# Performance work log

Hardware: AMD Instinct MI355X
Metric: run time of the kernel (lower is better)

## Reference

```python
import jax, jax.numpy as jnp
import numpy as np

DIM, HID, E, K = 512, 2048, 8, 2

def setup_inputs() -> dict:
    key = jax.random.key(0)
    ks = jax.random.split(key, 6)
    x = jax.random.normal(ks[0], (8, 4096, DIM), dtype=jnp.float32)
    assign = jax.random.randint(ks[1], (8, 4096, K), 0, E, dtype=jnp.int32)
    W1 = jax.random.normal(ks[2], (E, DIM, HID), dtype=jnp.float32) * 0.02
    b1 = jnp.zeros((E, HID), dtype=jnp.float32)
    W2 = jax.random.normal(ks[3], (E, HID, DIM), dtype=jnp.float32) * 0.02
    b2 = jnp.zeros((E, DIM), dtype=jnp.float32)
    return {"x": x, "assign": assign, "W1": W1, "b1": b1, "W2": W2, "b2": b2}

def reference(x, assign, W1, b1, W2, b2):
    # x: [B,S,D]; assign: [B,S,K] expert ids; hash router => uniform weights 1/K
    B, S, D = x.shape
    k = assign.shape[-1]
    num_experts = W1.shape[0]
    flat_x = x.reshape(B * S, D)
    flat_assign = assign.reshape(B * S, k)
    inv_k = jnp.asarray(1.0 / k, dtype=x.dtype)
    out = jnp.zeros((B * S, D), dtype=x.dtype)
    for e in range(num_experts):  # small fixed expert count
        # total routing weight for this expert per token (handles duplicate slots)
        token_w = (flat_assign == e).sum(-1).astype(x.dtype) * inv_k  # [B*S]
        h = jax.nn.relu(flat_x @ W1[e] + b1[e])        # [B*S, hidden]
        y = h @ W2[e] + b2[e]                          # [B*S, D]
        out = out + y * token_w[:, None]               # zero weight => zero contribution
    return out.reshape(B, S, D)
```

## Files before the change

kernel.cpp:

```cpp
#include <hip/hip_runtime.h>


#define NTOK 32768
#define DIM  512
#define HID  2048
#define NE   8
#define TM   64
#define MAXTILE 128

#define XBASE 0
#define HBASE 65536
#define RBASE 98304
#define LDS_BYTES 163840

typedef __attribute__((ext_vector_type(8))) short short8;
typedef __attribute__((ext_vector_type(4))) float f32x4;
typedef unsigned short ushort_t;

__device__ __forceinline__ unsigned short f2bf(float f) {
  union { float f; unsigned u; } v; v.f = f;
  unsigned r = v.u + 0x7FFFu + ((v.u >> 16) & 1u);
  return (unsigned short)(r >> 16);
}
__device__ __forceinline__ void g2l16(const void* g, void* l) {
  __builtin_amdgcn_global_load_lds(
      (const __attribute__((address_space(1))) void*)g,
      (__attribute__((address_space(3))) void*)l, 16, 0, 0);
}

#define SCHB __builtin_amdgcn_sched_barrier(0)
#define VMW4 do { asm volatile("s_waitcnt vmcnt(4)" ::: "memory"); SCHB; } while (0)
#define MFMA16(a, b, c) __builtin_amdgcn_mfma_f32_16x16x32_bf16(a, b, c, 0, 0, 0)

__device__ __forceinline__ void transp_body(const float* __restrict__ src,
                                            ushort_t* __restrict__ dst,
                                            int R, int C, int rb, int cb,
                                            int t, float tile[64][68]) {
  {
    const int tr = t >> 2, tc = (t & 3) * 16;
    const f32x4* s = (const f32x4*)(src + (size_t)(rb + tr) * C + cb + tc);
    f32x4 v0 = __builtin_nontemporal_load(s + 0);
    f32x4 v1 = __builtin_nontemporal_load(s + 1);
    f32x4 v2 = __builtin_nontemporal_load(s + 2);
    f32x4 v3 = __builtin_nontemporal_load(s + 3);
    *(f32x4*)&tile[tr][tc + 0]  = v0;
    *(f32x4*)&tile[tr][tc + 4]  = v1;
    *(f32x4*)&tile[tr][tc + 8]  = v2;
    *(f32x4*)&tile[tr][tc + 12] = v3;
  }
  __syncthreads();
  {
    const int n = t >> 2, ks = (t & 3) * 16;
    short8 o0, o1;
#pragma unroll
    for (int j = 0; j < 8; ++j) o0[j] = (short)f2bf(tile[ks + j][n]);
#pragma unroll
    for (int j = 0; j < 8; ++j) o1[j] = (short)f2bf(tile[ks + 8 + j][n]);
    ushort_t* d = dst + (size_t)(cb + n) * R + rb + ks;
    *(short8*)(d) = o0;
    *(short8*)(d + 8) = o1;
  }
}

__global__ __launch_bounds__(256) void moe_prep(
    const float* __restrict__ W1, const float* __restrict__ W2,
    ushort_t* __restrict__ W1b, ushort_t* __restrict__ W2b,
    const int* __restrict__ assign, int* __restrict__ cnt,
    int* __restrict__ lists) {
  __shared__ float tile[64][68];
  __shared__ int lcnt[NE], gbase[NE];
  const int b = blockIdx.x;
  const int t = threadIdx.x;
  if (b < 2048) {
    int e = b >> 8, rem = b & 255;
    int rb = (rem >> 5) * 64, cb = (rem & 31) * 64;
    transp_body(W1 + (size_t)e * DIM * HID, W1b + (size_t)e * HID * DIM,
                DIM, HID, rb, cb, t, tile);
  } else if (b < 4096) {
    int bb = b - 2048;
    int e = bb >> 8, rem = bb & 255;
    int rb = (rem >> 3) * 64, cb = (rem & 7) * 64;
    transp_body(W2 + (size_t)e * HID * DIM, W2b + (size_t)e * DIM * HID,
                HID, DIM, rb, cb, t, tile);
  } else {
    int tt = (b - 4096) * 256 + t;
    if (t < NE) lcnt[t] = 0;
    __syncthreads();
    int a0 = assign[2 * tt + 0];
    int a1 = assign[2 * tt + 1];
    int r0, r1 = -1;
    r0 = atomicAdd(&lcnt[a0], 1);
    if (a0 != a1) r1 = atomicAdd(&lcnt[a1], 1);
    __syncthreads();
    if (t < NE) gbase[t] = atomicAdd(&cnt[t], lcnt[t]);
    __syncthreads();
    if (a0 == a1) {
      lists[a0 * NTOK + gbase[a0] + r0] = tt | 0x10000;
    } else {
      lists[a0 * NTOK + gbase[a0] + r0] = tt;
      lists[a1 * NTOK + gbase[a1] + r1] = tt;
    }
  }
}

__global__ __launch_bounds__(512, 2) void moe_gemm(
    const float* __restrict__ x, const ushort_t* __restrict__ W1b,
    const float* __restrict__ b1, const ushort_t* __restrict__ W2b,
    const float* __restrict__ b2, const int* __restrict__ cnt,
    const int* __restrict__ lists, float* __restrict__ out) {
  extern __shared__ char smem[];

  const int id = blockIdx.x;
  const int e = id & 7;
  const int tile = id >> 3;
  const int n_e = cnt[e];
  const int t0 = tile * TM;
  if (t0 >= n_e) return;

  const int tid = threadIdx.x;
  const int wid = tid >> 6;
  const int lane = tid & 63;
  const int lr = lane & 15, lg = lane >> 4;
  const int lr7 = lr & 7;
  const int lrq = (lr >> 1) & 3;
  const int l3 = lane >> 3, l7 = lane & 7;

  char* const ring0 = smem + RBASE + wid * 8192;

  const ushort_t* gW1c = W1b + ((size_t)(e * HID) + wid * 32 + l3) * DIM + (l7 ^ l3) * 8;
  const ushort_t* gW2c = W2b + ((size_t)(e * DIM) + wid * 64 + (lane >> 2)) * HID +
                         ((lane & 3) ^ ((lane >> 3) & 3)) * 8;
  const float* b1e = b1 + (size_t)e * HID + wid * 32 + lr;

  auto IS_G1 = [&](const ushort_t* wb, int p, int half, int slot) {
    char* d = ring0 + slot * 2048 + lane * 16;
    const ushort_t* g = wb + (size_t)(half * 16) * DIM + p * 64;
    g2l16(g, d);
    g2l16(g + (size_t)8 * DIM, d + 1024);
  };
  auto IS_G2 = [&](const ushort_t* wb, int q, int h, int slot) {
    char* d = ring0 + slot * 2048 + lane * 16;
    const ushort_t* g = wb + (size_t)(h * 32) * HID + q * 32;
    g2l16(g, d);
    g2l16(g + (size_t)16 * HID, d + 1024);
  };

#define B1LOAD(d0, d1, BI) do { \
  const float* a_ = b1e + (BI) * 256; \
  asm volatile("global_load_dword %0, %2, off\n\t" \
               "global_load_dword %1, %2, off offset:64" \
               : "=&v"(d0), "=&v"(d1) : "v"(a_)); \
} while (0)

#define XRD(dst, mf, p, kf) do { \
  const int row_ = (mf) * 16 + lr; \
  const int u_ = (p) * 8 + (kf) * 4 + lg; \
  dst = *(const short8*)(smem + XBASE + row_ * 1024 + \
        ((u_ & ~7) | ((u_ & 7) ^ (row_ & 7))) * 16); } while (0)
#define HRD(dst, mf, q) do { \
  const int row_ = (mf) * 16 + lr; \
  const int u_ = (q) * 4 + lg; \
  dst = *(const short8*)(smem + HBASE + row_ * 512 + \
        ((u_ & ~7) | ((u_ & 7) ^ (row_ & 7))) * 16); } while (0)
#define W1RD(dst, S, kf) \
  dst = *(const short8*)(ring0 + (S) * 2048 + lr * 128 + ((((kf) * 4 + lg) ^ lr7) * 16))
#define W2RD(dst, S, half) \
  dst = *(const short8*)(ring0 + (S) * 2048 + ((half) * 16 + lr) * 64 + ((lg ^ lrq) * 16))

#define G1_PHASE(p, S0, S1, ISS) do { \
  VMW4; \
  short8 b00, b01, b10, b11; \
  W1RD(b00, S0, 0); W1RD(b10, S1, 0); W1RD(b01, S0, 1); W1RD(b11, S1, 1); \
  SCHB; \
  short8 x00, x01, x02, x03, x10, x11, x12, x13; \
  XRD(x00, 0, p, 0); XRD(x01, 1, p, 0); XRD(x02, 2, p, 0); XRD(x03, 3, p, 0); \
  XRD(x10, 0, p, 1); XRD(x11, 1, p, 1); XRD(x12, 2, p, 1); XRD(x13, 3, p, 1); \
  SCHB; \
  asm volatile("s_waitcnt lgkmcnt(8)" ::: "memory"); SCHB; \
  ISS; SCHB; \
  __builtin_amdgcn_s_setprio(1); \
  acc1[0][0] = MFMA16(x00, b00, acc1[0][0]); acc1[0][1] = MFMA16(x00, b10, acc1[0][1]); \
  acc1[1][0] = MFMA16(x01, b00, acc1[1][0]); acc1[1][1] = MFMA16(x01, b10, acc1[1][1]); \
  acc1[2][0] = MFMA16(x02, b00, acc1[2][0]); acc1[2][1] = MFMA16(x02, b10, acc1[2][1]); \
  acc1[3][0] = MFMA16(x03, b00, acc1[3][0]); acc1[3][1] = MFMA16(x03, b10, acc1[3][1]); \
  acc1[0][0] = MFMA16(x10, b01, acc1[0][0]); acc1[0][1] = MFMA16(x10, b11, acc1[0][1]); \
  acc1[1][0] = MFMA16(x11, b01, acc1[1][0]); acc1[1][1] = MFMA16(x11, b11, acc1[1][1]); \
  acc1[2][0] = MFMA16(x12, b01, acc1[2][0]); acc1[2][1] = MFMA16(x12, b11, acc1[2][1]); \
  acc1[3][0] = MFMA16(x13, b01, acc1[3][0]); acc1[3][1] = MFMA16(x13, b11, acc1[3][1]); \
  __builtin_amdgcn_s_setprio(0); SCHB; \
} while (0)

#define G2_PHASE(q, S0, S1, ISS) do { \
  VMW4; \
  short8 w0, w1, w2, w3; \
  W2RD(w0, S0, 0); W2RD(w1, S0, 1); W2RD(w2, S1, 0); W2RD(w3, S1, 1); \
  SCHB; \
  short8 h0, h1, h2, h3; \
  HRD(h0, 0, q); HRD(h1, 1, q); HRD(h2, 2, q); HRD(h3, 3, q); \
  SCHB; \
  asm volatile("s_waitcnt lgkmcnt(4)" ::: "memory"); SCHB; \
  ISS; SCHB; \
  __builtin_amdgcn_s_setprio(1); \
  acc2[0][0] = MFMA16(h0, w0, acc2[0][0]); acc2[0][1] = MFMA16(h0, w1, acc2[0][1]); \
  acc2[0][2] = MFMA16(h0, w2, acc2[0][2]); acc2[0][3] = MFMA16(h0, w3, acc2[0][3]); \
  acc2[1][0] = MFMA16(h1, w0, acc2[1][0]); acc2[1][1] = MFMA16(h1, w1, acc2[1][1]); \
  acc2[1][2] = MFMA16(h1, w2, acc2[1][2]); acc2[1][3] = MFMA16(h1, w3, acc2[1][3]); \
  acc2[2][0] = MFMA16(h2, w0, acc2[2][0]); acc2[2][1] = MFMA16(h2, w1, acc2[2][1]); \
  acc2[2][2] = MFMA16(h2, w2, acc2[2][2]); acc2[2][3] = MFMA16(h2, w3, acc2[2][3]); \
  acc2[3][0] = MFMA16(h3, w0, acc2[3][0]); acc2[3][1] = MFMA16(h3, w1, acc2[3][1]); \
  acc2[3][2] = MFMA16(h3, w2, acc2[3][2]); acc2[3][3] = MFMA16(h3, w3, acc2[3][3]); \
  __builtin_amdgcn_s_setprio(0); SCHB; \
} while (0)

#define HWRITE(B0v, B1v) do { \
  _Pragma("unroll") \
  for (int mf = 0; mf < 4; ++mf) \
    _Pragma("unroll") \
    for (int nf = 0; nf < 2; ++nf) \
      _Pragma("unroll") \
      for (int r = 0; r < 4; ++r) { \
        int m_ = mf * 16 + lg * 4 + r; \
        int col_ = wid * 32 + nf * 16 + lr; \
        float hv_ = fmaxf(acc1[mf][nf][r] + (nf ? (B1v) : (B0v)), 0.0f); \
        int u_ = col_ >> 3; \
        *(ushort_t*)(smem + HBASE + m_ * 512 + \
                     ((u_ & ~7) | ((u_ & 7) ^ (m_ & 7))) * 16 + \
                     (col_ & 7) * 2) = f2bf(hv_); \
      } \
} while (0)

#define CHUNK(C, BU0, BU1, BN0, BN1) do { \
  f32x4 acc1[4][2]; \
  _Pragma("unroll") \
  for (int i_ = 0; i_ < 4; ++i_) { \
    acc1[i_][0] = f32x4{0.f, 0.f, 0.f, 0.f}; \
    acc1[i_][1] = f32x4{0.f, 0.f, 0.f, 0.f}; \
  } \
  G1_PHASE(0, 0, 1, { B1LOAD(BN0, BN1, ((C) < 7 ? (C) + 1 : 7)); \
                      IS_G1(gW1c, 2, 0, 0); IS_G1(gW1c, 2, 1, 1); }); \
  G1_PHASE(1, 2, 3, { IS_G1(gW1c, 3, 0, 2); IS_G1(gW1c, 3, 1, 3); }); \
  G1_PHASE(2, 0, 1, { IS_G1(gW1c, 4, 0, 0); IS_G1(gW1c, 4, 1, 1); }); \
  G1_PHASE(3, 2, 3, { IS_G1(gW1c, 5, 0, 2); IS_G1(gW1c, 5, 1, 3); }); \
  G1_PHASE(4, 0, 1, { IS_G1(gW1c, 6, 0, 0); IS_G1(gW1c, 6, 1, 1); }); \
  G1_PHASE(5, 2, 3, { IS_G1(gW1c, 7, 0, 2); IS_G1(gW1c, 7, 1, 3); }); \
  G1_PHASE(6, 0, 1, { IS_G2(gW2c, 0, 0, 0); IS_G2(gW2c, 0, 1, 1); }); \
  G1_PHASE(7, 2, 3, { IS_G2(gW2c, 1, 0, 2); IS_G2(gW2c, 1, 1, 3); }); \
  asm volatile("s_waitcnt lgkmcnt(0)" ::: "memory"); \
  __builtin_amdgcn_s_barrier(); SCHB; \
  HWRITE(BU0, BU1); \
  SCHB; \
  asm volatile("s_waitcnt lgkmcnt(0)" ::: "memory"); \
  __builtin_amdgcn_s_barrier(); SCHB; \
  G2_PHASE(0, 0, 1, { IS_G2(gW2c, 2, 0, 0); IS_G2(gW2c, 2, 1, 1); }); \
  G2_PHASE(1, 2, 3, { IS_G2(gW2c, 3, 0, 2); IS_G2(gW2c, 3, 1, 3); }); \
  G2_PHASE(2, 0, 1, { IS_G2(gW2c, 4, 0, 0); IS_G2(gW2c, 4, 1, 1); }); \
  G2_PHASE(3, 2, 3, { IS_G2(gW2c, 5, 0, 2); IS_G2(gW2c, 5, 1, 3); }); \
  G2_PHASE(4, 0, 1, { IS_G2(gW2c, 6, 0, 0); IS_G2(gW2c, 6, 1, 1); }); \
  G2_PHASE(5, 2, 3, { IS_G2(gW2c, 7, 0, 2); IS_G2(gW2c, 7, 1, 3); }); \
  G2_PHASE(6, 0, 1, { IS_G1(gW1c + 131072, 0, 0, 0); IS_G1(gW1c + 131072, 0, 1, 1); }); \
  G2_PHASE(7, 2, 3, { IS_G1(gW1c + 131072, 1, 0, 2); IS_G1(gW1c + 131072, 1, 1, 3); }); \
  gW1c += 131072; gW2c += 256; \
} while (0)

  {
    int row = tid >> 3;
    int idx = t0 + row;
    int tok = lists[e * NTOK + (idx < n_e ? idx : 0)] & 0xFFFF;
    const float* xr = x + (size_t)tok * DIM;
#pragma unroll
    for (int i = 0; i < 8; ++i) {
      int u = (tid & 7) + 8 * i;
      f32x4 v0 = __builtin_nontemporal_load((const f32x4*)(xr + u * 8));
      f32x4 v1 = __builtin_nontemporal_load((const f32x4*)(xr + u * 8 + 4));
      short8 pk;
      pk[0] = (short)f2bf(v0.x); pk[1] = (short)f2bf(v0.y);
      pk[2] = (short)f2bf(v0.z); pk[3] = (short)f2bf(v0.w);
      pk[4] = (short)f2bf(v1.x); pk[5] = (short)f2bf(v1.y);
      pk[6] = (short)f2bf(v1.z); pk[7] = (short)f2bf(v1.w);
      int row8 = row & 7;
      int su = (u & ~7) | ((u & 7) ^ row8);
      *(short8*)(smem + XBASE + row * 1024 + su * 16) = pk;
    }
  }
  __syncthreads();

  float b1A0, b1A1, b1B0, b1B1;
  B1LOAD(b1A0, b1A1, 0);
  IS_G1(gW1c, 0, 0, 0); IS_G1(gW1c, 0, 1, 1);
  IS_G1(gW1c, 1, 0, 2); IS_G1(gW1c, 1, 1, 3);
  SCHB;

  f32x4 acc2[4][4];
#pragma unroll
  for (int i = 0; i < 4; ++i)
#pragma unroll
    for (int j = 0; j < 4; ++j) acc2[i][j] = f32x4{0.f, 0.f, 0.f, 0.f};

#pragma unroll 1
  for (int cc = 0; cc < 4; ++cc) {
    const int c0 = cc * 2;
    CHUNK(c0,     b1A0, b1A1, b1B0, b1B1);
    CHUNK(c0 + 1, b1B0, b1B1, b1A0, b1A1);
  }
  asm volatile("s_waitcnt vmcnt(0)" ::: "memory");
  SCHB;
  asm volatile("" :: "v"(b1A0), "v"(b1A1));

  float b2v[4];
#pragma unroll
  for (int nf = 0; nf < 4; ++nf)
    b2v[nf] = b2[e * DIM + wid * 64 + nf * 16 + lr];

#pragma unroll
  for (int mf = 0; mf < 4; ++mf)
#pragma unroll
    for (int r = 0; r < 4; ++r) {
      int m = mf * 16 + lg * 4 + r;
      int gi = t0 + m;
      if (gi >= n_e) continue;
      int ent = lists[e * NTOK + gi];
      int t = ent & 0xFFFF;
      float w = (ent & 0x10000) ? 1.0f : 0.5f;
      float* orow = out + (size_t)t * DIM;
#pragma unroll
      for (int nf = 0; nf < 4; ++nf) {
        int col = wid * 64 + nf * 16 + lr;
        atomicAdd(orow + col, (acc2[mf][nf][r] + b2v[nf]) * w);
      }
    }
}

extern "C" void kernel_launch(void* const* d_in, const int* in_sizes, int n_in,
                              void* d_out, int out_size, void* d_ws, size_t ws_size,
                              hipStream_t stream) {
  const float* x      = (const float*)d_in[0];
  const int*   assign = (const int*)d_in[1];
  const float* W1     = (const float*)d_in[2];
  const float* b1     = (const float*)d_in[3];
  const float* W2     = (const float*)d_in[4];
  const float* b2     = (const float*)d_in[5];
  float* out = (float*)d_out;

  char* ws = (char*)d_ws;
  int* cnt   = (int*)ws;
  int* lists = (int*)(ws + 1024);
  ushort_t* W1b = (ushort_t*)(ws + (2ull << 20));
  ushort_t* W2b = (ushort_t*)(ws + (2ull << 20) + 18874368ull);

  (void)hipMemsetAsync(d_out, 0, (size_t)out_size * sizeof(float), stream);
  (void)hipMemsetAsync(cnt, 0, 256, stream);

  moe_prep<<<4096 + NTOK / 256, 256, 0, stream>>>(W1, W2, W1b, W2b,
                                                  assign, cnt, lists);

  (void)hipFuncSetAttribute((const void*)moe_gemm,
                            hipFuncAttributeMaxDynamicSharedMemorySize, LDS_BYTES);
  moe_gemm<<<NE * MAXTILE, 512, LDS_BYTES, stream>>>(x, W1b, b1, W2b, b2,
                                                     cnt, lists, out);
}
```

Baseline: 398.2 us.

## Replace atomic output scatter with per-slot bf16 buffer and combine kernel

The GEMM epilogue no longer does fp32 atomicAdd into the output. Each token's result is written as bf16 into one of two slot buffers, chosen by a new bit recorded in the routing lists, and a separate combine kernel averages the two slots into the output. The MFMA operands are swapped so accumulators come out transposed, which allows vectorized bias loads and packed 4-element stores for both H and Y. This removes the output memset and the atomic traffic, but adds a bf16 round-trip of the expert outputs (a precision loss), an extra kernel launch, and launch_bounds is changed to one block per SM.

New measurement: 355.4 us. 1.12x faster.

```diff
diff --git a/kernel.cpp b/kernel.cpp
--- a/kernel.cpp
+++ b/kernel.cpp
@@ -15,12 +15,17 @@
 
 typedef __attribute__((ext_vector_type(8))) short short8;
 typedef __attribute__((ext_vector_type(4))) float f32x4;
+typedef __attribute__((ext_vector_type(4))) unsigned short us4b;
 typedef unsigned short ushort_t;
 
 __device__ __forceinline__ unsigned short f2bf(float f) {
   union { float f; unsigned u; } v; v.f = f;
   unsigned r = v.u + 0x7FFFu + ((v.u >> 16) & 1u);
   return (unsigned short)(r >> 16);
+}
+__device__ __forceinline__ float bf2f(unsigned short s) {
+  union { unsigned u; float f; } v; v.u = ((unsigned)s) << 16;
+  return v.f;
 }
 __device__ __forceinline__ void g2l16(const void* g, void* l) {
   __builtin_amdgcn_global_load_lds(
@@ -98,16 +103,32 @@
       lists[a0 * NTOK + gbase[a0] + r0] = tt | 0x10000;
     } else {
       lists[a0 * NTOK + gbase[a0] + r0] = tt;
-      lists[a1 * NTOK + gbase[a1] + r1] = tt;
+      lists[a1 * NTOK + gbase[a1] + r1] = tt | (1 << 17);
     }
   }
 }
 
-__global__ __launch_bounds__(512, 2) void moe_gemm(
+__global__ __launch_bounds__(256) void moe_combine(
+    const ushort_t* __restrict__ Yb, float* __restrict__ out) {
+  size_t i = ((size_t)blockIdx.x * 256 + threadIdx.x) * 8;
+  short8 y0 = *(const short8*)(Yb + i);
+  short8 y1 = *(const short8*)(Yb + (size_t)NTOK * DIM + i);
+  f32x4 o0, o1;
+#pragma unroll
+  for (int j = 0; j < 4; ++j)
+    o0[j] = 0.5f * (bf2f((unsigned short)y0[j]) + bf2f((unsigned short)y1[j]));
+#pragma unroll
+  for (int j = 0; j < 4; ++j)
+    o1[j] = 0.5f * (bf2f((unsigned short)y0[4 + j]) + bf2f((unsigned short)y1[4 + j]));
+  *(f32x4*)(out + i) = o0;
+  *(f32x4*)(out + i + 4) = o1;
+}
+
+__global__ __launch_bounds__(512, 1) void moe_gemm(
     const float* __restrict__ x, const ushort_t* __restrict__ W1b,
     const float* __restrict__ b1, const ushort_t* __restrict__ W2b,
     const float* __restrict__ b2, const int* __restrict__ cnt,
-    const int* __restrict__ lists, float* __restrict__ out) {
+    const int* __restrict__ lists, ushort_t* __restrict__ Yb) {
   extern __shared__ char smem[];
 
   const int id = blockIdx.x;
@@ -130,7 +151,7 @@
   const ushort_t* gW1c = W1b + ((size_t)(e * HID) + wid * 32 + l3) * DIM + (l7 ^ l3) * 8;
   const ushort_t* gW2c = W2b + ((size_t)(e * DIM) + wid * 64 + (lane >> 2)) * HID +
                          ((lane & 3) ^ ((lane >> 3) & 3)) * 8;
-  const float* b1e = b1 + (size_t)e * HID + wid * 32 + lr;
+  const float* b1e = b1 + (size_t)e * HID + wid * 32 + lg * 4;
 
   auto IS_G1 = [&](const ushort_t* wb, int p, int half, int slot) {
     char* d = ring0 + slot * 2048 + lane * 16;
@@ -147,18 +168,18 @@
 
 #define B1LOAD(d0, d1, BI) do { \
   const float* a_ = b1e + (BI) * 256; \
-  asm volatile("global_load_dword %0, %2, off\n\t" \
-               "global_load_dword %1, %2, off offset:64" \
+  asm volatile("global_load_dwordx4 %0, %2, off\n\t" \
+               "global_load_dwordx4 %1, %2, off offset:64" \
                : "=&v"(d0), "=&v"(d1) : "v"(a_)); \
 } while (0)
 
-#define XRD(dst, mf, p, kf) do { \
-  const int row_ = (mf) * 16 + lr; \
+#define XRD(dst, nf, p, kf) do { \
+  const int row_ = (nf) * 16 + lr; \
   const int u_ = (p) * 8 + (kf) * 4 + lg; \
   dst = *(const short8*)(smem + XBASE + row_ * 1024 + \
         ((u_ & ~7) | ((u_ & 7) ^ (row_ & 7))) * 16); } while (0)
-#define HRD(dst, mf, q) do { \
-  const int row_ = (mf) * 16 + lr; \
+#define HRD(dst, nf, q) do { \
+  const int row_ = (nf) * 16 + lr; \
   const int u_ = (q) * 4 + lg; \
   dst = *(const short8*)(smem + HBASE + row_ * 512 + \
         ((u_ & ~7) | ((u_ & 7) ^ (row_ & 7))) * 16); } while (0)
@@ -169,8 +190,8 @@
 
 #define G1_PHASE(p, S0, S1, ISS) do { \
   VMW4; \
-  short8 b00, b01, b10, b11; \
-  W1RD(b00, S0, 0); W1RD(b10, S1, 0); W1RD(b01, S0, 1); W1RD(b11, S1, 1); \
+  short8 wa0k0, wa1k0, wa0k1, wa1k1; \
+  W1RD(wa0k0, S0, 0); W1RD(wa1k0, S1, 0); W1RD(wa0k1, S0, 1); W1RD(wa1k1, S1, 1); \
   SCHB; \
   short8 x00, x01, x02, x03, x10, x11, x12, x13; \
   XRD(x00, 0, p, 0); XRD(x01, 1, p, 0); XRD(x02, 2, p, 0); XRD(x03, 3, p, 0); \
@@ -179,14 +200,14 @@
   asm volatile("s_waitcnt lgkmcnt(8)" ::: "memory"); SCHB; \
   ISS; SCHB; \
   __builtin_amdgcn_s_setprio(1); \
-  acc1[0][0] = MFMA16(x00, b00, acc1[0][0]); acc1[0][1] = MFMA16(x00, b10, acc1[0][1]); \
-  acc1[1][0] = MFMA16(x01, b00, acc1[1][0]); acc1[1][1] = MFMA16(x01, b10, acc1[1][1]); \
-  acc1[2][0] = MFMA16(x02, b00, acc1[2][0]); acc1[2][1] = MFMA16(x02, b10, acc1[2][1]); \
-  acc1[3][0] = MFMA16(x03, b00, acc1[3][0]); acc1[3][1] = MFMA16(x03, b10, acc1[3][1]); \
-  acc1[0][0] = MFMA16(x10, b01, acc1[0][0]); acc1[0][1] = MFMA16(x10, b11, acc1[0][1]); \
-  acc1[1][0] = MFMA16(x11, b01, acc1[1][0]); acc1[1][1] = MFMA16(x11, b11, acc1[1][1]); \
-  acc1[2][0] = MFMA16(x12, b01, acc1[2][0]); acc1[2][1] = MFMA16(x12, b11, acc1[2][1]); \
-  acc1[3][0] = MFMA16(x13, b01, acc1[3][0]); acc1[3][1] = MFMA16(x13, b11, acc1[3][1]); \
+  acc1[0][0] = MFMA16(wa0k0, x00, acc1[0][0]); acc1[1][0] = MFMA16(wa1k0, x00, acc1[1][0]); \
+  acc1[0][1] = MFMA16(wa0k0, x01, acc1[0][1]); acc1[1][1] = MFMA16(wa1k0, x01, acc1[1][1]); \
+  acc1[0][2] = MFMA16(wa0k0, x02, acc1[0][2]); acc1[1][2] = MFMA16(wa1k0, x02, acc1[1][2]); \
+  acc1[0][3] = MFMA16(wa0k0, x03, acc1[0][3]); acc1[1][3] = MFMA16(wa1k0, x03, acc1[1][3]); \
+  acc1[0][0] = MFMA16(wa0k1, x10, acc1[0][0]); acc1[1][0] = MFMA16(wa1k1, x10, acc1[1][0]); \
+  acc1[0][1] = MFMA16(wa0k1, x11, acc1[0][1]); acc1[1][1] = MFMA16(wa1k1, x11, acc1[1][1]); \
+  acc1[0][2] = MFMA16(wa0k1, x12, acc1[0][2]); acc1[1][2] = MFMA16(wa1k1, x12, acc1[1][2]); \
+  acc1[0][3] = MFMA16(wa0k1, x13, acc1[0][3]); acc1[1][3] = MFMA16(wa1k1, x13, acc1[1][3]); \
   __builtin_amdgcn_s_setprio(0); SCHB; \
 } while (0)
 
@@ -201,41 +222,43 @@
   asm volatile("s_waitcnt lgkmcnt(4)" ::: "memory"); SCHB; \
   ISS; SCHB; \
   __builtin_amdgcn_s_setprio(1); \
-  acc2[0][0] = MFMA16(h0, w0, acc2[0][0]); acc2[0][1] = MFMA16(h0, w1, acc2[0][1]); \
-  acc2[0][2] = MFMA16(h0, w2, acc2[0][2]); acc2[0][3] = MFMA16(h0, w3, acc2[0][3]); \
-  acc2[1][0] = MFMA16(h1, w0, acc2[1][0]); acc2[1][1] = MFMA16(h1, w1, acc2[1][1]); \
-  acc2[1][2] = MFMA16(h1, w2, acc2[1][2]); acc2[1][3] = MFMA16(h1, w3, acc2[1][3]); \
-  acc2[2][0] = MFMA16(h2, w0, acc2[2][0]); acc2[2][1] = MFMA16(h2, w1, acc2[2][1]); \
-  acc2[2][2] = MFMA16(h2, w2, acc2[2][2]); acc2[2][3] = MFMA16(h2, w3, acc2[2][3]); \
-  acc2[3][0] = MFMA16(h3, w0, acc2[3][0]); acc2[3][1] = MFMA16(h3, w1, acc2[3][1]); \
-  acc2[3][2] = MFMA16(h3, w2, acc2[3][2]); acc2[3][3] = MFMA16(h3, w3, acc2[3][3]); \
+  acc2[0][0] = MFMA16(w0, h0, acc2[0][0]); acc2[0][1] = MFMA16(w0, h1, acc2[0][1]); \
+  acc2[0][2] = MFMA16(w0, h2, acc2[0][2]); acc2[0][3] = MFMA16(w0, h3, acc2[0][3]); \
+  acc2[1][0] = MFMA16(w1, h0, acc2[1][0]); acc2[1][1] = MFMA16(w1, h1, acc2[1][1]); \
+  acc2[1][2] = MFMA16(w1, h2, acc2[1][2]); acc2[1][3] = MFMA16(w1, h3, acc2[1][3]); \
+  acc2[2][0] = MFMA16(w2, h0, acc2[2][0]); acc2[2][1] = MFMA16(w2, h1, acc2[2][1]); \
+  acc2[2][2] = MFMA16(w2, h2, acc2[2][2]); acc2[2][3] = MFMA16(w2, h3, acc2[2][3]); \
+  acc2[3][0] = MFMA16(w3, h0, acc2[3][0]); acc2[3][1] = MFMA16(w3, h1, acc2[3][1]); \
+  acc2[3][2] = MFMA16(w3, h2, acc2[3][2]); acc2[3][3] = MFMA16(w3, h3, acc2[3][3]); \
   __builtin_amdgcn_s_setprio(0); SCHB; \
 } while (0)
 
-#define HWRITE(B0v, B1v) do { \
+#define HWRITE(Q0, Q1) do { \
   _Pragma("unroll") \
-  for (int mf = 0; mf < 4; ++mf) \
+  for (int mf_ = 0; mf_ < 2; ++mf_) { \
+    f32x4 bq_ = mf_ ? (Q1) : (Q0); \
+    int hl_ = wid * 32 + mf_ * 16 + lg * 4; \
+    int u_ = hl_ >> 3; \
     _Pragma("unroll") \
-    for (int nf = 0; nf < 2; ++nf) \
-      _Pragma("unroll") \
-      for (int r = 0; r < 4; ++r) { \
-        int m_ = mf * 16 + lg * 4 + r; \
-        int col_ = wid * 32 + nf * 16 + lr; \
-        float hv_ = fmaxf(acc1[mf][nf][r] + (nf ? (B1v) : (B0v)), 0.0f); \
-        int u_ = col_ >> 3; \
-        *(ushort_t*)(smem + HBASE + m_ * 512 + \
-                     ((u_ & ~7) | ((u_ & 7) ^ (m_ & 7))) * 16 + \
-                     (col_ & 7) * 2) = f2bf(hv_); \
-      } \
+    for (int nf_ = 0; nf_ < 4; ++nf_) { \
+      int tokr_ = nf_ * 16 + lr; \
+      us4b pk_; \
+      pk_.x = f2bf(fmaxf(acc1[mf_][nf_][0] + bq_[0], 0.0f)); \
+      pk_.y = f2bf(fmaxf(acc1[mf_][nf_][1] + bq_[1], 0.0f)); \
+      pk_.z = f2bf(fmaxf(acc1[mf_][nf_][2] + bq_[2], 0.0f)); \
+      pk_.w = f2bf(fmaxf(acc1[mf_][nf_][3] + bq_[3], 0.0f)); \
+      int u2_ = (u_ & ~7) | ((u_ & 7) ^ (tokr_ & 7)); \
+      *(us4b*)(smem + HBASE + tokr_ * 512 + u2_ * 16 + (lg & 1) * 8) = pk_; \
+    } \
+  } \
 } while (0)
 
 #define CHUNK(C, BU0, BU1, BN0, BN1) do { \
-  f32x4 acc1[4][2]; \
+  f32x4 acc1[2][4]; \
   _Pragma("unroll") \
-  for (int i_ = 0; i_ < 4; ++i_) { \
-    acc1[i_][0] = f32x4{0.f, 0.f, 0.f, 0.f}; \
-    acc1[i_][1] = f32x4{0.f, 0.f, 0.f, 0.f}; \
-  } \
+  for (int i_ = 0; i_ < 2; ++i_) \
+    _Pragma("unroll") \
+    for (int j_ = 0; j_ < 4; ++j_) acc1[i_][j_] = f32x4{0.f, 0.f, 0.f, 0.f}; \
   G1_PHASE(0, 0, 1, { B1LOAD(BN0, BN1, ((C) < 7 ? (C) + 1 : 7)); \
                       IS_G1(gW1c, 2, 0, 0); IS_G1(gW1c, 2, 1, 1); }); \
   G1_PHASE(1, 2, 3, { IS_G1(gW1c, 3, 0, 2); IS_G1(gW1c, 3, 1, 3); }); \
@@ -277,14 +300,13 @@
       pk[2] = (short)f2bf(v0.z); pk[3] = (short)f2bf(v0.w);
       pk[4] = (short)f2bf(v1.x); pk[5] = (short)f2bf(v1.y);
       pk[6] = (short)f2bf(v1.z); pk[7] = (short)f2bf(v1.w);
-      int row8 = row & 7;
-      int su = (u & ~7) | ((u & 7) ^ row8);
+      int su = (u & ~7) | ((u & 7) ^ (row & 7));
       *(short8*)(smem + XBASE + row * 1024 + su * 16) = pk;
     }
   }
   __syncthreads();
 
-  float b1A0, b1A1, b1B0, b1B1;
+  f32x4 b1A0, b1A1, b1B0, b1B1;
   B1LOAD(b1A0, b1A1, 0);
   IS_G1(gW1c, 0, 0, 0); IS_G1(gW1c, 0, 1, 1);
   IS_G1(gW1c, 1, 0, 2); IS_G1(gW1c, 1, 1, 3);
@@ -306,28 +328,29 @@
   SCHB;
   asm volatile("" :: "v"(b1A0), "v"(b1A1));
 
-  float b2v[4];
-#pragma unroll
-  for (int nf = 0; nf < 4; ++nf)
-    b2v[nf] = b2[e * DIM + wid * 64 + nf * 16 + lr];
-
+  f32x4 b2q[4];
 #pragma unroll
   for (int mf = 0; mf < 4; ++mf)
-#pragma unroll
-    for (int r = 0; r < 4; ++r) {
-      int m = mf * 16 + lg * 4 + r;
-      int gi = t0 + m;
-      if (gi >= n_e) continue;
-      int ent = lists[e * NTOK + gi];
-      int t = ent & 0xFFFF;
-      float w = (ent & 0x10000) ? 1.0f : 0.5f;
-      float* orow = out + (size_t)t * DIM;
-#pragma unroll
-      for (int nf = 0; nf < 4; ++nf) {
-        int col = wid * 64 + nf * 16 + lr;
-        atomicAdd(orow + col, (acc2[mf][nf][r] + b2v[nf]) * w);
-      }
+    b2q[mf] = *(const f32x4*)(b2 + e * DIM + wid * 64 + mf * 16 + lg * 4);
+
+#pragma unroll
+  for (int nf = 0; nf < 4; ++nf) {
+    int gi = t0 + nf * 16 + lr;
+    if (gi >= n_e) continue;
+    int ent = lists[e * NTOK + gi];
+    int tok = ent & 0xFFFF;
+    int slot = (ent >> 17) & 1;
+    size_t base = ((size_t)(slot * NTOK + tok)) * DIM + wid * 64 + lg * 4;
+#pragma unroll
+    for (int mf = 0; mf < 4; ++mf) {
+      f32x4 y = acc2[mf][nf] + b2q[mf];
+      us4b pk;
+      pk.x = f2bf(y[0]); pk.y = f2bf(y[1]); pk.z = f2bf(y[2]); pk.w = f2bf(y[3]);
+      *(us4b*)(Yb + base + mf * 16) = pk;
+      if (ent & 0x10000)
+        *(us4b*)(Yb + base + (size_t)NTOK * DIM + mf * 16) = pk;
     }
+  }
 }
 
 extern "C" void kernel_launch(void* const* d_in, const int* in_sizes, int n_in,
@@ -346,8 +369,8 @@
   int* lists = (int*)(ws + 1024);
   ushort_t* W1b = (ushort_t*)(ws + (2ull << 20));
   ushort_t* W2b = (ushort_t*)(ws + (2ull << 20) + 18874368ull);
-
-  (void)hipMemsetAsync(d_out, 0, (size_t)out_size * sizeof(float), stream);
+  ushort_t* Yb  = (ushort_t*)(ws + (2ull << 20) + 2ull * 18874368ull);
+
   (void)hipMemsetAsync(cnt, 0, 256, stream);
 
   moe_prep<<<4096 + NTOK / 256, 256, 0, stream>>>(W1, W2, W1b, W2b,
@@ -356,5 +379,7 @@
   (void)hipFuncSetAttribute((const void*)moe_gemm,
                             hipFuncAttributeMaxDynamicSharedMemorySize, LDS_BYTES);
   moe_gemm<<<NE * MAXTILE, 512, LDS_BYTES, stream>>>(x, W1b, b1, W2b, b2,
-                                                     cnt, lists, out);
-}
+                                                     cnt, lists, Yb);
+
+  moe_combine<<<NTOK * DIM / 2048, 256, 0, stream>>>(Yb, out);
+}
```
